# Optimization experiments

Hardware: AMD Instinct MI355X
Metric: run time of the kernel (lower is better)

## Reference

```python
import jax, jax.numpy as jnp
import numpy as np

N_LAYER = 4
N_HEAD = 12
D_MODEL = 768
SEQ_LEN = 2048
VOCAB = 50257
BATCH = 2


def _sinusoid_pe(seq_len, d_model):
    pos = np.arange(seq_len, dtype=np.float32)[:, None]
    div = np.exp(np.arange(0, d_model, 2, dtype=np.float32) * (-np.log(10000.0) / d_model))
    pe = np.zeros((seq_len, d_model), dtype=np.float32)
    pe[:, 0::2] = np.sin(pos * div)
    pe[:, 1::2] = np.cos(pos * div)
    return jnp.asarray(pe[None])  # [1, C, D]


def setup_inputs() -> dict:
    key = jax.random.key(0)
    ks = jax.random.split(key, 12)
    s = 0.02
    return {
        "features": jax.random.randint(ks[0], (BATCH, SEQ_LEN), 0, VOCAB),
        "targets": jax.random.randint(ks[1], (BATCH, SEQ_LEN), 0, VOCAB),
        "tok_embed": jax.random.normal(ks[2], (VOCAB, D_MODEL), jnp.float32) * s,
        "pos_emb": _sinusoid_pe(SEQ_LEN, D_MODEL),
        "ln1_w": jnp.ones((N_LAYER, D_MODEL), jnp.float32),
        "ln1_b": jnp.zeros((N_LAYER, D_MODEL), jnp.float32),
        "attn_w": jax.random.normal(ks[3], (N_LAYER, D_MODEL, 3 * D_MODEL), jnp.float32) * s,
        "attn_b": jnp.zeros((N_LAYER, 3 * D_MODEL), jnp.float32),
        "proj_w": jax.random.normal(ks[4], (N_LAYER, D_MODEL, D_MODEL), jnp.float32) * s,
        "proj_b": jnp.zeros((N_LAYER, D_MODEL), jnp.float32),
        "ln2_w": jnp.ones((N_LAYER, D_MODEL), jnp.float32),
        "ln2_b": jnp.zeros((N_LAYER, D_MODEL), jnp.float32),
        "ffn_w1": jax.random.normal(ks[5], (N_LAYER, D_MODEL, 4 * D_MODEL), jnp.float32) * s,
        "ffn_b1": jnp.zeros((N_LAYER, 4 * D_MODEL), jnp.float32),
        "ffn_w2": jax.random.normal(ks[6], (N_LAYER, 4 * D_MODEL, D_MODEL), jnp.float32) * s,
        "ffn_b2": jnp.zeros((N_LAYER, D_MODEL), jnp.float32),
        "lnf_w": jnp.ones((D_MODEL,), jnp.float32),
        "lnf_b": jnp.zeros((D_MODEL,), jnp.float32),
        "final_w": jax.random.normal(ks[7], (D_MODEL, VOCAB), jnp.float32) * s,
    }


def _layernorm(x, w, b, eps=1e-5):
    mu = jnp.mean(x, axis=-1, keepdims=True)
    var = jnp.var(x, axis=-1, keepdims=True)
    return (x - mu) * jax.lax.rsqrt(var + eps) * w + b


def _attention(x, wqkv, bqkv, wo, bo):
    B, C, E = x.shape
    dh = E // N_HEAD
    qkv = x @ wqkv + bqkv  # [B, C, 3E]
    q, k, v = jnp.split(qkv, 3, axis=-1)
    q = q.reshape(B, C, N_HEAD, dh)
    k = k.reshape(B, C, N_HEAD, dh)
    v = v.reshape(B, C, N_HEAD, dh)
    att = jnp.einsum("bqhd,bkhd->bhqk", q, k) / jnp.sqrt(jnp.float32(dh))
    causal = jnp.tril(jnp.ones((C, C), bool))
    att = jnp.where(causal, att, -jnp.inf)
    att = jax.nn.softmax(att, axis=-1)
    y = jnp.einsum("bhqk,bkhd->bqhd", att, v).reshape(B, C, E)
    return y @ wo + bo


def reference(features, targets, tok_embed, pos_emb, ln1_w, ln1_b, attn_w, attn_b,
              proj_w, proj_b, ln2_w, ln2_b, ffn_w1, ffn_b1, ffn_w2, ffn_b2,
              lnf_w, lnf_b, final_w):
    C = features.shape[1]
    x = tok_embed[features] + pos_emb[:, :C]
    for l in range(N_LAYER):
        h = _layernorm(x, ln1_w[l], ln1_b[l])
        x = x + _attention(h, attn_w[l], attn_b[l], proj_w[l], proj_b[l])
        h = _layernorm(x, ln2_w[l], ln2_b[l])
        h = jax.nn.gelu(h @ ffn_w1[l] + ffn_b1[l], approximate=False) @ ffn_w2[l] + ffn_b2[l]
        x = x + h
    x = _layernorm(x, lnf_w, lnf_b)
    logits = x @ final_w  # [B, C, V]
    logp = jax.nn.log_softmax(logits, axis=-1)
    tgt = targets.reshape(-1)
    valid = tgt != -1
    tgt_safe = jnp.where(valid, tgt, 0)
    nll = -jnp.take_along_axis(logp.reshape(-1, logits.shape[-1]), tgt_safe[:, None], axis=1)[:, 0]
    loss = jnp.sum(jnp.where(valid, nll, 0.0)) / jnp.maximum(jnp.sum(valid), 1)
    return logits, loss
```

## Files before the change

kernel.cpp:

```cpp
#include <hip/hip_runtime.h>
#include <math.h>

#define N_LAYER 4
#define N_HEAD  12
#define D_MODEL 768
#define SEQ     2048
#define VOCAB   50257
#define BATCH   2
#define MROWS   (BATCH*SEQ)

typedef __bf16 bf16;
typedef __bf16 bf16x8 __attribute__((ext_vector_type(8)));
typedef float  f32x4  __attribute__((ext_vector_type(4)));
typedef short  short8v __attribute__((ext_vector_type(8)));

__global__ __launch_bounds__(256) void embed_kernel(
    const int* __restrict__ feat, const float* __restrict__ tok,
    const float* __restrict__ pos, float* __restrict__ x)
{
    int row = blockIdx.x;
    int cpos = row & (SEQ - 1);
    int tid = feat[row];
    const float* te = tok + (size_t)tid * D_MODEL;
    const float* pe = pos + (size_t)cpos * D_MODEL;
    float* xr = x + (size_t)row * D_MODEL;
    for (int c = threadIdx.x; c < D_MODEL; c += 256)
        xr[c] = te[c] + pe[c];
}

__global__ __launch_bounds__(256) void ln_kernel(
    const float* __restrict__ x, const float* __restrict__ w,
    const float* __restrict__ b, bf16* __restrict__ out)
{
    int row = blockIdx.x;
    const float* xr = x + (size_t)row * D_MODEL;
    float lv[3];
    float s = 0.f, ss = 0.f;
#pragma unroll
    for (int i = 0; i < 3; i++) {
        float v = xr[threadIdx.x + i * 256];
        lv[i] = v; s += v; ss += v * v;
    }
#pragma unroll
    for (int o = 32; o; o >>= 1) { s += __shfl_down(s, o, 64); ss += __shfl_down(ss, o, 64); }
    __shared__ float red[8];
    int wid = threadIdx.x >> 6;
    if ((threadIdx.x & 63) == 0) { red[wid] = s; red[wid + 4] = ss; }
    __syncthreads();
    s  = red[0] + red[1] + red[2] + red[3];
    ss = red[4] + red[5] + red[6] + red[7];
    float mu  = s * (1.f / D_MODEL);
    float var = ss * (1.f / D_MODEL) - mu * mu;
    float rs  = rsqrtf(var + 1e-5f);
#pragma unroll
    for (int i = 0; i < 3; i++) {
        int c = threadIdx.x + i * 256;
        out[(size_t)row * D_MODEL + c] = (bf16)((lv[i] - mu) * rs * w[c] + b[c]);
    }
}

__global__ __launch_bounds__(256) void transpose_conv_kernel(
    const float* __restrict__ W, bf16* __restrict__ Wt, int K, int N)
{
    int l = blockIdx.z;
    const float* Wl = W + (size_t)l * K * N;
    bf16* Wtl = Wt + (size_t)l * K * N;
    __shared__ float tile[32][33];
    int k0 = blockIdx.y * 32, n0 = blockIdx.x * 32;
    for (int idx = threadIdx.x; idx < 1024; idx += 256) {
        int i = idx >> 5, j = idx & 31;
        int n = n0 + j;
        tile[i][j] = (n < N) ? Wl[(size_t)(k0 + i) * N + n] : 0.f;
    }
    __syncthreads();
    for (int idx = threadIdx.x; idx < 1024; idx += 256) {
        int j = idx >> 5, i = idx & 31;
        int n = n0 + j;
        if (n < N) Wtl[(size_t)n * K + k0 + i] = (bf16)tile[i][j];
    }
}

template<bool BIAS, bool GELU_, int OUTM>
__global__ __launch_bounds__(256) void gemm_kernel(
    const bf16* __restrict__ A, const bf16* __restrict__ Bt,
    const float* __restrict__ bias, void* __restrict__ Cout,
    int M, int N, int K)
{
    __shared__ bf16 As[128][40];
    __shared__ bf16 Bs[128][40];
    int tid = threadIdx.x;
    int lane = tid & 63, wid = tid >> 6;
    int wr = (wid >> 1) * 64, wc = (wid & 1) * 64;
    int row0 = blockIdx.x * 128, col0 = blockIdx.y * 128;
    f32x4 acc[4][4] = {};

    for (int k0 = 0; k0 < K; k0 += 32) {
        __syncthreads();
#pragma unroll
        for (int t = 0; t < 2; t++) {
            int c = tid + t * 256;
            int r = c >> 2, ko = (c & 3) * 8;
            *(short8v*)&As[r][ko] = *(const short8v*)&A[(size_t)(row0 + r) * K + k0 + ko];
            int n = col0 + r; if (n >= N) n = N - 1;
            *(short8v*)&Bs[r][ko] = *(const short8v*)&Bt[(size_t)n * K + k0 + ko];
        }
        __syncthreads();
        int fr = lane & 15, fg = (lane >> 4) * 8;
        bf16x8 af[4], bfr[4];
#pragma unroll
        for (int m = 0; m < 4; m++) af[m] = *(const bf16x8*)&As[wr + m * 16 + fr][fg];
#pragma unroll
        for (int n = 0; n < 4; n++) bfr[n] = *(const bf16x8*)&Bs[wc + n * 16 + fr][fg];
#pragma unroll
        for (int m = 0; m < 4; m++)
#pragma unroll
            for (int n = 0; n < 4; n++)
                acc[m][n] = __builtin_amdgcn_mfma_f32_16x16x32_bf16(af[m], bfr[n], acc[m][n], 0, 0, 0);
    }

    int fr = lane & 15, g = lane >> 4;
#pragma unroll
    for (int m = 0; m < 4; m++) {
#pragma unroll
        for (int n = 0; n < 4; n++) {
            int col = col0 + wc + n * 16 + fr;
            if (col >= N) continue;
            float bv = BIAS ? bias[col] : 0.f;
#pragma unroll
            for (int r = 0; r < 4; r++) {
                int row = row0 + wr + m * 16 + g * 4 + r;
                float v = acc[m][n][r] + bv;
                if (GELU_) v = 0.5f * v * (1.f + erff(v * 0.70710678118f));
                if (OUTM == 0)      ((float*)Cout)[(size_t)row * N + col] = v;
                else if (OUTM == 1) ((bf16*)Cout)[(size_t)row * N + col] = (bf16)v;
                else                ((float*)Cout)[(size_t)row * N + col] += v;
            }
        }
    }
}

__global__ __launch_bounds__(256) void attn_kernel(
    const bf16* __restrict__ qkv, bf16* __restrict__ y)
{
    int qt = blockIdx.x, h = blockIdx.y, b = blockIdx.z;
    int q0 = qt * 64;
    const size_t rs = 3 * D_MODEL;
    const bf16* qbase = qkv + (size_t)b * SEQ * rs + h * 64;
    const bf16* kbase = qbase + D_MODEL;
    const bf16* vbase = qbase + 2 * D_MODEL;
    __shared__ bf16 Qs[64][72];
    __shared__ bf16 Ks[64][72];
    __shared__ bf16 Vts[64][72];
    __shared__ bf16 Ps[64][72];
    int tid = threadIdx.x, lane = tid & 63, wid = tid >> 6;
    int fr = lane & 15, g = lane >> 4;

#pragma unroll
    for (int t = 0; t < 2; t++) {
        int c = tid + t * 256; int r = c >> 3, ko = (c & 7) * 8;
        *(short8v*)&Qs[r][ko] = *(const short8v*)&qbase[(size_t)(q0 + r) * rs + ko];
    }

    f32x4 acco[4] = {};
    float mrow[4], lrow[4];
#pragma unroll
    for (int r = 0; r < 4; r++) { mrow[r] = -1e30f; lrow[r] = 0.f; }

    for (int j0 = 0; j0 <= q0; j0 += 64) {
        __syncthreads();
#pragma unroll
        for (int t = 0; t < 2; t++) {
            int c = tid + t * 256; int r = c >> 3, ko = (c & 7) * 8;
            *(short8v*)&Ks[r][ko] = *(const short8v*)&kbase[(size_t)(j0 + r) * rs + ko];
            short8v vv = *(const short8v*)&vbase[(size_t)(j0 + r) * rs + ko];
            bf16 vb[8]; *(short8v*)vb = vv;
#pragma unroll
            for (int e = 0; e < 8; e++) Vts[ko + e][r] = vb[e];
        }
        __syncthreads();

        f32x4 accs[4] = {};
        bf16x8 aq[2];
#pragma unroll
        for (int kk = 0; kk < 2; kk++) aq[kk] = *(const bf16x8*)&Qs[wid * 16 + fr][kk * 32 + g * 8];
#pragma unroll
        for (int n = 0; n < 4; n++)
#pragma unroll
            for (int kk = 0; kk < 2; kk++) {
                bf16x8 bk = *(const bf16x8*)&Ks[n * 16 + fr][kk * 32 + g * 8];
                accs[n] = __builtin_amdgcn_mfma_f32_16x16x32_bf16(aq[kk], bk, accs[n], 0, 0, 0);
            }

        bool diag = (j0 == q0);
#pragma unroll
        for (int n = 0; n < 4; n++) {
            int jc = j0 + n * 16 + fr;
#pragma unroll
            for (int r = 0; r < 4; r++) {
                float sv = accs[n][r] * 0.125f;
                if (diag) { int irow = q0 + wid * 16 + g * 4 + r; if (jc > irow) sv = -1e30f; }
                accs[n][r] = sv;
            }
        }

        float pscale[4];
#pragma unroll
        for (int r = 0; r < 4; r++) {
            float pm = fmaxf(fmaxf(accs[0][r], accs[1][r]), fmaxf(accs[2][r], accs[3][r]));
#pragma unroll
            for (int o = 1; o < 16; o <<= 1) pm = fmaxf(pm, __shfl_xor(pm, o, 64));
            float mnew = fmaxf(mrow[r], pm);
            float corr = __expf(mrow[r] - mnew);
            mrow[r] = mnew;
            float ls = 0.f;
#pragma unroll
            for (int n = 0; n < 4; n++) {
                float p = __expf(accs[n][r] - mnew);
                accs[n][r] = p; ls += p;
            }
#pragma unroll
            for (int o = 1; o < 16; o <<= 1) ls += __shfl_xor(ls, o, 64);
            lrow[r] = lrow[r] * corr + ls;
            pscale[r] = corr;
        }
#pragma unroll
        for (int n = 0; n < 4; n++)
#pragma unroll
            for (int r = 0; r < 4; r++) acco[n][r] *= pscale[r];

#pragma unroll
        for (int n = 0; n < 4; n++)
#pragma unroll
            for (int r = 0; r < 4; r++)
                Ps[wid * 16 + g * 4 + r][n * 16 + fr] = (bf16)accs[n][r];

#pragma unroll
        for (int kk = 0; kk < 2; kk++) {
            bf16x8 ap = *(const bf16x8*)&Ps[wid * 16 + fr][kk * 32 + g * 8];
#pragma unroll
            for (int n = 0; n < 4; n++) {
                bf16x8 bv = *(const bf16x8*)&Vts[n * 16 + fr][kk * 32 + g * 8];
                acco[n] = __builtin_amdgcn_mfma_f32_16x16x32_bf16(ap, bv, acco[n], 0, 0, 0);
            }
        }
    }

    bf16* yb = y + (size_t)b * SEQ * D_MODEL + h * 64;
#pragma unroll
    for (int n = 0; n < 4; n++)
#pragma unroll
        for (int r = 0; r < 4; r++) {
            int row = q0 + wid * 16 + g * 4 + r;
            yb[(size_t)row * D_MODEL + n * 16 + fr] = (bf16)(acco[n][r] / lrow[r]);
        }
}

__global__ __launch_bounds__(256) void loss_row_kernel(
    const float* __restrict__ logits, const int* __restrict__ tgt, float* __restrict__ accum)
{
    int row = blockIdx.x;
    const float* lr = logits + (size_t)row * VOCAB;
    float m = -1e30f, s = 0.f;
    for (int c = threadIdx.x; c < VOCAB; c += 256) {
        float v = lr[c];
        float mn = fmaxf(m, v);
        s = s * __expf(m - mn) + __expf(v - mn);
        m = mn;
    }
#pragma unroll
    for (int o = 1; o < 64; o <<= 1) {
        float mo = __shfl_xor(m, o, 64);
        float so = __shfl_xor(s, o, 64);
        float mn = fmaxf(m, mo);
        s = s * __expf(m - mn) + so * __expf(mo - mn);
        m = mn;
    }
    __shared__ float sm[4], ssv[4];
    int lane = threadIdx.x & 63, wid = threadIdx.x >> 6;
    if (lane == 0) { sm[wid] = m; ssv[wid] = s; }
    __syncthreads();
    if (threadIdx.x == 0) {
        float M0 = sm[0], S0 = ssv[0];
        for (int w = 1; w < 4; w++) {
            float mn = fmaxf(M0, sm[w]);
            S0 = S0 * __expf(M0 - mn) + ssv[w] * __expf(sm[w] - mn);
            M0 = mn;
        }
        float lse = M0 + logf(S0);
        int t = tgt[row];
        if (t >= 0) {
            atomicAdd(accum, lse - lr[t]);
            atomicAdd(accum + 1, 1.f);
        }
    }
}

__global__ void loss_final_kernel(const float* __restrict__ accum, float* __restrict__ out)
{
    out[0] = accum[0] / fmaxf(accum[1], 1.f);
}

extern "C" void kernel_launch(void* const* d_in, const int* in_sizes, int n_in,
                              void* d_out, int out_size, void* d_ws, size_t ws_size,
                              hipStream_t stream)
{
    const int*   feat  = (const int*)d_in[0];
    const int*   tgt   = (const int*)d_in[1];
    const float* tok   = (const float*)d_in[2];
    const float* pos   = (const float*)d_in[3];
    const float* ln1w  = (const float*)d_in[4];
    const float* ln1b  = (const float*)d_in[5];
    const float* attnw = (const float*)d_in[6];
    const float* attnb = (const float*)d_in[7];
    const float* projw = (const float*)d_in[8];
    const float* projb = (const float*)d_in[9];
    const float* ln2w  = (const float*)d_in[10];
    const float* ln2b  = (const float*)d_in[11];
    const float* fw1   = (const float*)d_in[12];
    const float* fb1   = (const float*)d_in[13];
    const float* fw2   = (const float*)d_in[14];
    const float* fb2   = (const float*)d_in[15];
    const float* lnfw  = (const float*)d_in[16];
    const float* lnfb  = (const float*)d_in[17];
    const float* finw  = (const float*)d_in[18];

    char* ws = (char*)d_ws;
    size_t off = 0;
    auto alloc = [&](size_t bytes) -> void* {
        void* p = ws + off; off += (bytes + 255) & ~(size_t)255; return p;
    };
    float* x     = (float*)alloc((size_t)MROWS * D_MODEL * 4);
    bf16*  h     = (bf16*) alloc((size_t)MROWS * D_MODEL * 2);
    bf16*  big   = (bf16*) alloc((size_t)MROWS * 4 * D_MODEL * 2);
    bf16*  ybuf  = (bf16*) alloc((size_t)MROWS * D_MODEL * 2);
    bf16*  awt   = (bf16*) alloc((size_t)N_LAYER * 3 * D_MODEL * D_MODEL * 2);
    bf16*  pwt   = (bf16*) alloc((size_t)N_LAYER * D_MODEL * D_MODEL * 2);
    bf16*  f1wt  = (bf16*) alloc((size_t)N_LAYER * 4 * D_MODEL * D_MODEL * 2);
    bf16*  f2wt  = (bf16*) alloc((size_t)N_LAYER * 4 * D_MODEL * D_MODEL * 2);
    bf16*  fwt   = (bf16*) alloc((size_t)VOCAB * D_MODEL * 2);
    float* accum = (float*)alloc(256);

    float* logits = (float*)d_out;
    float* lossp  = (float*)d_out + (size_t)MROWS * VOCAB;

    dim3 blk(256);
    transpose_conv_kernel<<<dim3(3 * D_MODEL / 32, D_MODEL / 32, N_LAYER), blk, 0, stream>>>(attnw, awt, D_MODEL, 3 * D_MODEL);
    transpose_conv_kernel<<<dim3(D_MODEL / 32, D_MODEL / 32, N_LAYER), blk, 0, stream>>>(projw, pwt, D_MODEL, D_MODEL);
    transpose_conv_kernel<<<dim3(4 * D_MODEL / 32, D_MODEL / 32, N_LAYER), blk, 0, stream>>>(fw1, f1wt, D_MODEL, 4 * D_MODEL);
    transpose_conv_kernel<<<dim3(D_MODEL / 32, 4 * D_MODEL / 32, N_LAYER), blk, 0, stream>>>(fw2, f2wt, 4 * D_MODEL, D_MODEL);
    transpose_conv_kernel<<<dim3((VOCAB + 31) / 32, D_MODEL / 32, 1), blk, 0, stream>>>(finw, fwt, D_MODEL, VOCAB);

    embed_kernel<<<MROWS, blk, 0, stream>>>(feat, tok, pos, x);

    for (int l = 0; l < N_LAYER; l++) {
        ln_kernel<<<MROWS, blk, 0, stream>>>(x, ln1w + l * D_MODEL, ln1b + l * D_MODEL, h);
        gemm_kernel<true, false, 1><<<dim3(MROWS / 128, (3 * D_MODEL) / 128), blk, 0, stream>>>(
            h, awt + (size_t)l * 3 * D_MODEL * D_MODEL, attnb + l * 3 * D_MODEL, big,
            MROWS, 3 * D_MODEL, D_MODEL);
        attn_kernel<<<dim3(SEQ / 64, N_HEAD, BATCH), blk, 0, stream>>>(big, ybuf);
        gemm_kernel<true, false, 2><<<dim3(MROWS / 128, D_MODEL / 128), blk, 0, stream>>>(
            ybuf, pwt + (size_t)l * D_MODEL * D_MODEL, projb + l * D_MODEL, x,
            MROWS, D_MODEL, D_MODEL);
        ln_kernel<<<MROWS, blk, 0, stream>>>(x, ln2w + l * D_MODEL, ln2b + l * D_MODEL, h);
        gemm_kernel<true, true, 1><<<dim3(MROWS / 128, (4 * D_MODEL) / 128), blk, 0, stream>>>(
            h, f1wt + (size_t)l * 4 * D_MODEL * D_MODEL, fb1 + l * 4 * D_MODEL, big,
            MROWS, 4 * D_MODEL, D_MODEL);
        gemm_kernel<true, false, 2><<<dim3(MROWS / 128, D_MODEL / 128), blk, 0, stream>>>(
            big, f2wt + (size_t)l * 4 * D_MODEL * D_MODEL, fb2 + l * D_MODEL, x,
            MROWS, D_MODEL, 4 * D_MODEL);
    }

    ln_kernel<<<MROWS, blk, 0, stream>>>(x, lnfw, lnfb, h);
    gemm_kernel<false, false, 0><<<dim3(MROWS / 128, (VOCAB + 127) / 128), blk, 0, stream>>>(
        h, fwt, nullptr, logits, MROWS, VOCAB, D_MODEL);

    hipMemsetAsync(accum, 0, 8, stream);
    loss_row_kernel<<<MROWS, blk, 0, stream>>>(logits, tgt, accum);
    loss_final_kernel<<<1, 1, 0, stream>>>(accum, lossp);

    (void)in_sizes; (void)n_in; (void)out_size; (void)ws_size;
}
```

Before: 2.467 ms.

## Use direct global-to-LDS loads in GEMM, XCD swizzle, vectorize loss reads

The GEMM tile loads now use global_load_lds to write straight into shared memory without staging through registers, with an unpadded 32-wide LDS layout. The vocab-projection GEMM also remaps block IDs so neighbouring tiles land on the same XCD for better L2 reuse. The loss row kernel reads logits as aligned float4 with scalar head and tail handling. Dropping the LDS padding may bring back bank conflicts on the fragment reads, and the loads are still not double-buffered.

```diff
diff --git a/kernel.cpp b/kernel.cpp
--- a/kernel.cpp
+++ b/kernel.cpp
@@ -13,6 +13,13 @@
 typedef __bf16 bf16x8 __attribute__((ext_vector_type(8)));
 typedef float  f32x4  __attribute__((ext_vector_type(4)));
 typedef short  short8v __attribute__((ext_vector_type(8)));
+
+__device__ __forceinline__ void gload16(const bf16* g, const bf16* l) {
+    __builtin_amdgcn_global_load_lds(
+        (const __attribute__((address_space(1))) void*)g,
+        (__attribute__((address_space(3))) void*)l,
+        16, 0, 0);
+}
 
 __global__ __launch_bounds__(256) void embed_kernel(
     const int* __restrict__ feat, const float* __restrict__ tok,
@@ -80,37 +87,59 @@
     }
 }
 
-template<bool BIAS, bool GELU_, int OUTM>
+template<bool BIAS, bool GELU_, int OUTM, bool SWZ>
 __global__ __launch_bounds__(256) void gemm_kernel(
     const bf16* __restrict__ A, const bf16* __restrict__ Bt,
     const float* __restrict__ bias, void* __restrict__ Cout,
     int M, int N, int K)
 {
-    __shared__ bf16 As[128][40];
-    __shared__ bf16 Bs[128][40];
+    __shared__ __align__(16) bf16 As[128 * 32];
+    __shared__ __align__(16) bf16 Bs[128 * 32];
     int tid = threadIdx.x;
     int lane = tid & 63, wid = tid >> 6;
+
+    int nbx = gridDim.x;
+    int bid = blockIdx.y * nbx + blockIdx.x;
+    if (SWZ) {
+        int nwg = nbx * gridDim.y;
+        int q = nwg >> 3, r = nwg & 7;
+        int xcd = bid & 7, loc = bid >> 3;
+        bid = (xcd < r ? xcd * (q + 1) : r * (q + 1) + (xcd - r) * q) + loc;
+    }
+    int row0 = (bid % nbx) * 128;
+    int col0 = (bid / nbx) * 128;
+
     int wr = (wid >> 1) * 64, wc = (wid & 1) * 64;
-    int row0 = blockIdx.x * 128, col0 = blockIdx.y * 128;
+
+    int srow = wid * 16 + (lane >> 2);
+    int selem = (lane & 3) * 8;
+    const bf16* Ab0 = A + (size_t)(row0 + srow) * K + selem;
+    const bf16* Ab1 = Ab0 + (size_t)64 * K;
+    int bn0 = col0 + srow;      if (bn0 >= N) bn0 = N - 1;
+    int bn1 = col0 + srow + 64; if (bn1 >= N) bn1 = N - 1;
+    const bf16* Bb0 = Bt + (size_t)bn0 * K + selem;
+    const bf16* Bb1 = Bt + (size_t)bn1 * K + selem;
+    bf16* ldsA0 = As + wid * 512;
+    bf16* ldsA1 = As + (wid + 4) * 512;
+    bf16* ldsB0 = Bs + wid * 512;
+    bf16* ldsB1 = Bs + (wid + 4) * 512;
+
     f32x4 acc[4][4] = {};
+    int fr = lane & 15, fg8 = (lane >> 4) * 8;
 
     for (int k0 = 0; k0 < K; k0 += 32) {
+        if (k0) __syncthreads();
+        gload16(Ab0 + k0, ldsA0);
+        gload16(Ab1 + k0, ldsA1);
+        gload16(Bb0 + k0, ldsB0);
+        gload16(Bb1 + k0, ldsB1);
         __syncthreads();
-#pragma unroll
-        for (int t = 0; t < 2; t++) {
-            int c = tid + t * 256;
-            int r = c >> 2, ko = (c & 3) * 8;
-            *(short8v*)&As[r][ko] = *(const short8v*)&A[(size_t)(row0 + r) * K + k0 + ko];
-            int n = col0 + r; if (n >= N) n = N - 1;
-            *(short8v*)&Bs[r][ko] = *(const short8v*)&Bt[(size_t)n * K + k0 + ko];
-        }
-        __syncthreads();
-        int fr = lane & 15, fg = (lane >> 4) * 8;
+
         bf16x8 af[4], bfr[4];
 #pragma unroll
-        for (int m = 0; m < 4; m++) af[m] = *(const bf16x8*)&As[wr + m * 16 + fr][fg];
-#pragma unroll
-        for (int n = 0; n < 4; n++) bfr[n] = *(const bf16x8*)&Bs[wc + n * 16 + fr][fg];
+        for (int m = 0; m < 4; m++) af[m] = *(const bf16x8*)&As[(wr + m * 16 + fr) * 32 + fg8];
+#pragma unroll
+        for (int n = 0; n < 4; n++) bfr[n] = *(const bf16x8*)&Bs[(wc + n * 16 + fr) * 32 + fg8];
 #pragma unroll
         for (int m = 0; m < 4; m++)
 #pragma unroll
@@ -118,7 +147,7 @@
                 acc[m][n] = __builtin_amdgcn_mfma_f32_16x16x32_bf16(af[m], bfr[n], acc[m][n], 0, 0, 0);
     }
 
-    int fr = lane & 15, g = lane >> 4;
+    int g = lane >> 4;
 #pragma unroll
     for (int m = 0; m < 4; m++) {
 #pragma unroll
@@ -260,8 +289,24 @@
 {
     int row = blockIdx.x;
     const float* lr = logits + (size_t)row * VOCAB;
+    uintptr_t p = (uintptr_t)lr;
+    int lead = (int)((16 - (p & 15)) >> 2) & 3;
     float m = -1e30f, s = 0.f;
-    for (int c = threadIdx.x; c < VOCAB; c += 256) {
+    if ((int)threadIdx.x < lead) {
+        float v = lr[threadIdx.x];
+        m = v; s = 1.f;
+    }
+    int nvec = (VOCAB - lead) >> 2;
+    const float4* v4 = (const float4*)(lr + lead);
+    for (int i = threadIdx.x; i < nvec; i += 256) {
+        float4 v = v4[i];
+        float lm = fmaxf(fmaxf(v.x, v.y), fmaxf(v.z, v.w));
+        float mn = fmaxf(m, lm);
+        s = s * __expf(m - mn) + __expf(v.x - mn) + __expf(v.y - mn)
+          + __expf(v.z - mn) + __expf(v.w - mn);
+        m = mn;
+    }
+    for (int c = lead + nvec * 4 + threadIdx.x; c < VOCAB; c += 256) {
         float v = lr[c];
         float mn = fmaxf(m, v);
         s = s * __expf(m - mn) + __expf(v - mn);
@@ -354,24 +399,24 @@
 
     for (int l = 0; l < N_LAYER; l++) {
         ln_kernel<<<MROWS, blk, 0, stream>>>(x, ln1w + l * D_MODEL, ln1b + l * D_MODEL, h);
-        gemm_kernel<true, false, 1><<<dim3(MROWS / 128, (3 * D_MODEL) / 128), blk, 0, stream>>>(
+        gemm_kernel<true, false, 1, false><<<dim3(MROWS / 128, (3 * D_MODEL) / 128), blk, 0, stream>>>(
             h, awt + (size_t)l * 3 * D_MODEL * D_MODEL, attnb + l * 3 * D_MODEL, big,
             MROWS, 3 * D_MODEL, D_MODEL);
         attn_kernel<<<dim3(SEQ / 64, N_HEAD, BATCH), blk, 0, stream>>>(big, ybuf);
-        gemm_kernel<true, false, 2><<<dim3(MROWS / 128, D_MODEL / 128), blk, 0, stream>>>(
+        gemm_kernel<true, false, 2, false><<<dim3(MROWS / 128, D_MODEL / 128), blk, 0, stream>>>(
             ybuf, pwt + (size_t)l * D_MODEL * D_MODEL, projb + l * D_MODEL, x,
             MROWS, D_MODEL, D_MODEL);
         ln_kernel<<<MROWS, blk, 0, stream>>>(x, ln2w + l * D_MODEL, ln2b + l * D_MODEL, h);
-        gemm_kernel<true, true, 1><<<dim3(MROWS / 128, (4 * D_MODEL) / 128), blk, 0, stream>>>(
+        gemm_kernel<true, true, 1, false><<<dim3(MROWS / 128, (4 * D_MODEL) / 128), blk, 0, stream>>>(
             h, f1wt + (size_t)l * 4 * D_MODEL * D_MODEL, fb1 + l * 4 * D_MODEL, big,
             MROWS, 4 * D_MODEL, D_MODEL);
-        gemm_kernel<true, false, 2><<<dim3(MROWS / 128, D_MODEL / 128), blk, 0, stream>>>(
+        gemm_kernel<true, false, 2, false><<<dim3(MROWS / 128, D_MODEL / 128), blk, 0, stream>>>(
             big, f2wt + (size_t)l * 4 * D_MODEL * D_MODEL, fb2 + l * D_MODEL, x,
             MROWS, D_MODEL, 4 * D_MODEL);
     }
 
     ln_kernel<<<MROWS, blk, 0, stream>>>(x, lnfw, lnfb, h);
-    gemm_kernel<false, false, 0><<<dim3(MROWS / 128, (VOCAB + 127) / 128), blk, 0, stream>>>(
+    gemm_kernel<false, false, 0, true><<<dim3(MROWS / 128, (VOCAB + 127) / 128), blk, 0, stream>>>(
         h, fwt, nullptr, logits, MROWS, VOCAB, D_MODEL);
 
     hipMemsetAsync(accum, 0, 8, stream);
```

Measured after the change: 2.307 ms. 1.07x faster.
